# Kernel tuning notes

Measured on AMD Instinct MI355X. Metric: run time of the kernel, lower is better.

## Reference

```python
import jax, jax.numpy as jnp
import numpy as np

N = 16                      # input_dim (state dimension)
EPS = 1e-6
TRIL_R, TRIL_C = np.tril_indices(N)   # 136 lower-triangular slots


def setup_inputs() -> dict:
    key = jax.random.key(0)
    ks = jax.random.split(key, 7)
    B = 131072
    def xavier(k, fan_in, fan_out):
        lim = float(np.sqrt(6.0 / (fan_in + fan_out)))
        return jax.random.uniform(k, (fan_in, fan_out), jnp.float32, -lim, lim)
    return {
        "points": jax.random.normal(ks[0], (B, N), jnp.float32),
        "W0": xavier(ks[1], N, 512),
        "b0": jax.random.normal(ks[2], (512,), jnp.float32) * 0.01,
        "W1": xavier(ks[3], 512, 512),
        "b1": jax.random.normal(ks[4], (512,), jnp.float32) * 0.01,
        "W2": xavier(ks[5], 512, 136),
        "b2": jax.random.normal(ks[6], (136,), jnp.float32) * 0.01,
    }


def reference(points, W0, b0, W1, b1, W2, b2):
    # MLP: tanh, tanh, identity
    h = jnp.tanh(points @ W0 + b0)
    h = jnp.tanh(h @ W1 + b1)
    net = h @ W2 + b2                         # [B, 136] tril entries
    B = points.shape[0]
    # Batched scatter into lower-triangular matrices M: [B, N, N]
    M = jnp.zeros((B, N, N), points.dtype).at[:, TRIL_R, TRIL_C].set(net)
    # x^T (M M^T) x == ||M^T x||^2
    y = jnp.einsum('bij,bi->bj', M, points)   # (M^T x)_j = sum_i M_ij x_i
    vals = jnp.sum(y * y, axis=-1) + EPS * jnp.sum(points * points, axis=-1)
    return vals.reshape(-1, 1)
```

## Files before the change

kernel.cpp:

```cpp
#include <hip/hip_runtime.h>

typedef __bf16 bf16x4 __attribute__((ext_vector_type(4)));
typedef __bf16 bf16x8 __attribute__((ext_vector_type(8)));
typedef float f32x16 __attribute__((ext_vector_type(16)));

#define TC 2.885390081777926f

#define W0F_OFF 0
#define W1F_OFF 8192
#define W2F_OFF (8192 + 262144)

__global__ void prep_weights(const float* __restrict__ W0,
                             const float* __restrict__ W1,
                             const float* __restrict__ W2,
                             __bf16* __restrict__ ws) {
    const int wave = blockIdx.x * 8 + (threadIdx.x >> 6);
    const int l   = threadIdx.x & 63;
    const int col = l & 31, kh = l >> 5;
    const float* src; int nt, kk, S, nlim; float scl;
    if (wave < 16)       { src = W0; nt = wave; kk = 0;      S = 512; nlim = 512; scl = TC; }
    else if (wave < 528) { int r = wave - 16;  src = W1; nt = r >> 5; kk = r & 31; S = 512; nlim = 512; scl = TC; }
    else                 { int r = wave - 528; src = W2; nt = r >> 5; kk = r & 31; S = 136; nlim = 136; scl = 1.0f; }
    const int n  = nt * 32 + col;
    const int k0 = kk * 16 + kh * 8;
    bf16x8 v;
#pragma unroll
    for (int j = 0; j < 8; ++j)
        v[j] = (n < nlim) ? (__bf16)(src[(k0 + j) * S + n] * scl) : (__bf16)0.0f;
    *(bf16x8*)(ws + wave * 512 + l * 8) = v;
}

__device__ __forceinline__ float fast_tanh_pre(float y) {
#if __has_builtin(__builtin_amdgcn_exp2f)
    float e = __builtin_amdgcn_exp2f(y);
#else
    float e = exp2f(y);
#endif
    return 1.0f - 2.0f * __builtin_amdgcn_rcpf(e + 1.0f);
}

#define HSTR 520
#define NSTR 140

__global__ __launch_bounds__(512, 2)
void fused_mlp_quad(const float* __restrict__ points,
                    const float* __restrict__ b0,
                    const float* __restrict__ b1,
                    const float* __restrict__ b2,
                    const __bf16* __restrict__ ws,
                    float* __restrict__ out) {
    __shared__ __align__(16) unsigned char lds_raw[66560];
    __bf16* h  = (__bf16*)lds_raw;
    float* net = (float*)lds_raw;

    {
        const unsigned d = (blockIdx.x < 512)
                         ? ((blockIdx.x * 2654435761u) >> 29) : 0u;
        if (d > 0) __builtin_amdgcn_s_sleep(64);
        if (d > 1) __builtin_amdgcn_s_sleep(64);
        if (d > 2) __builtin_amdgcn_s_sleep(64);
        if (d > 3) __builtin_amdgcn_s_sleep(64);
        if (d > 4) __builtin_amdgcn_s_sleep(64);
        if (d > 5) __builtin_amdgcn_s_sleep(64);
        if (d > 6) __builtin_amdgcn_s_sleep(64);
    }

    const __bf16* w0f = ws + W0F_OFF;
    const __bf16* w1f = ws + W1F_OFF;
    const __bf16* w2f = ws + W2F_OFF;

    const int tid = threadIdx.x;
    const int w   = tid >> 6;
    const int l   = tid & 63;
    const int ln  = l & 31;
    const int hi  = l >> 5;
    const int row0 = blockIdx.x * 64;

    const int lofs = l * 8;
    const int ofs16 = (blockIdx.x >> 3) & 15;
    const int ofs8  = (blockIdx.x >> 3) & 7;

    {
        bf16x8 bx[2];
#pragma unroll
        for (int bt = 0; bt < 2; ++bt) {
            const float* src = points + (row0 + bt * 32 + ln) * 16 + hi * 8;
            float4 p0 = ((const float4*)src)[0];
            float4 p1 = ((const float4*)src)[1];
            bf16x8 v;
            v[0] = (__bf16)p0.x; v[1] = (__bf16)p0.y; v[2] = (__bf16)p0.z; v[3] = (__bf16)p0.w;
            v[4] = (__bf16)p1.x; v[5] = (__bf16)p1.y; v[6] = (__bf16)p1.z; v[7] = (__bf16)p1.w;
            bx[bt] = v;
        }
#pragma unroll
        for (int t = 0; t < 2; ++t) {
            const int ntg = w * 2 + t;
            bf16x8 wf = *(const bf16x8*)(w0f + ntg * 512 + lofs);
#pragma unroll
            for (int bt = 0; bt < 2; ++bt) {
                f32x16 acc = {};
                acc = __builtin_amdgcn_mfma_f32_32x32x16_bf16(wf, bx[bt], acc, 0, 0, 0);
#pragma unroll
                for (int rg = 0; rg < 4; ++rg) {
                    const int n0 = ntg * 32 + 8 * rg + 4 * hi;
                    float4 bias = *(const float4*)(b0 + n0);
                    bf16x4 v;
                    v[0] = (__bf16)fast_tanh_pre(fmaf(TC, bias.x, acc[4 * rg + 0]));
                    v[1] = (__bf16)fast_tanh_pre(fmaf(TC, bias.y, acc[4 * rg + 1]));
                    v[2] = (__bf16)fast_tanh_pre(fmaf(TC, bias.z, acc[4 * rg + 2]));
                    v[3] = (__bf16)fast_tanh_pre(fmaf(TC, bias.w, acc[4 * rg + 3]));
                    *(bf16x4*)(h + (bt * 32 + ln) * HSTR + n0) = v;
                }
            }
        }
    }
    __syncthreads();

    f32x16 acc1[2][2] = {};
    {
        const __bf16* arow0 = h + ln * HSTR + hi * 8;
        const __bf16* arow1 = h + (32 + ln) * HSTR + hi * 8;
        const __bf16* wb0 = w1f + (w * 2 + 0) * 16384 + lofs;
        const __bf16* wb1 = w1f + (w * 2 + 1) * 16384 + lofs;
        for (int ks2 = 0; ks2 < 16; ++ks2) {
            const int ks = (ks2 + ofs16) & 15;
            bf16x8 aa[2][2], bb[2][2];
#pragma unroll
            for (int u = 0; u < 2; ++u) {
                const int kk = ks * 2 + u;
                const int vo = kk * 512;
                aa[u][0] = *(const bf16x8*)(arow0 + kk * 16);
                aa[u][1] = *(const bf16x8*)(arow1 + kk * 16);
                bb[u][0] = *(const bf16x8*)(wb0 + vo);
                bb[u][1] = *(const bf16x8*)(wb1 + vo);
            }
#pragma unroll
            for (int u = 0; u < 2; ++u) {
#pragma unroll
                for (int t = 0; t < 2; ++t) {
                    acc1[0][t] = __builtin_amdgcn_mfma_f32_32x32x16_bf16(bb[u][t], aa[u][0], acc1[0][t], 0, 0, 0);
                    acc1[1][t] = __builtin_amdgcn_mfma_f32_32x32x16_bf16(bb[u][t], aa[u][1], acc1[1][t], 0, 0, 0);
                }
            }
        }
    }
    __syncthreads();
#pragma unroll
    for (int t = 0; t < 2; ++t) {
#pragma unroll
        for (int bt = 0; bt < 2; ++bt) {
#pragma unroll
            for (int rg = 0; rg < 4; ++rg) {
                const int n0 = (w * 2 + t) * 32 + 8 * rg + 4 * hi;
                float4 bias = *(const float4*)(b1 + n0);
                bf16x4 v;
                v[0] = (__bf16)fast_tanh_pre(fmaf(TC, bias.x, acc1[bt][t][4 * rg + 0]));
                v[1] = (__bf16)fast_tanh_pre(fmaf(TC, bias.y, acc1[bt][t][4 * rg + 1]));
                v[2] = (__bf16)fast_tanh_pre(fmaf(TC, bias.z, acc1[bt][t][4 * rg + 2]));
                v[3] = (__bf16)fast_tanh_pre(fmaf(TC, bias.w, acc1[bt][t][4 * rg + 3]));
                *(bf16x4*)(h + (bt * 32 + ln) * HSTR + n0) = v;
            }
        }
    }
    __syncthreads();

    f32x16 acc2a = {}, acc2e = {};
    const int nt2 = w >> 1;
    const int bt2 = w & 1;
    const bool two = (w < 2);
    {
        const __bf16* arowA = h + (bt2 * 32 + ln) * HSTR + hi * 8;
        const __bf16* arowE = h + ((w & 1) * 32 + ln) * HSTR + hi * 8;
        const __bf16* wbA = w2f + nt2 * 16384 + lofs;
        const __bf16* wbE = w2f + 4 * 16384 + lofs;
        for (int ks2 = 0; ks2 < 8; ++ks2) {
            const int ks = (ks2 + ofs8) & 7;
            bf16x8 aaA[2], wA[2], aaE[2], wE[2];
#pragma unroll
            for (int u = 0; u < 2; ++u) {
                const int kk = ks * 4 + u * 2;
                const int vo = kk * 512;
                aaA[u] = *(const bf16x8*)(arowA + kk * 16);
                wA[u]  = *(const bf16x8*)(wbA + vo);
                if (two) {
                    aaE[u] = *(const bf16x8*)(arowE + kk * 16);
                    wE[u]  = *(const bf16x8*)(wbE + vo);
                }
            }
            bf16x8 aaA2[2], wA2[2], aaE2[2], wE2[2];
#pragma unroll
            for (int u = 0; u < 2; ++u) {
                const int kk = ks * 4 + u * 2 + 1;
                const int vo = kk * 512;
                aaA2[u] = *(const bf16x8*)(arowA + kk * 16);
                wA2[u]  = *(const bf16x8*)(wbA + vo);
                if (two) {
                    aaE2[u] = *(const bf16x8*)(arowE + kk * 16);
                    wE2[u]  = *(const bf16x8*)(wbE + vo);
                }
            }
#pragma unroll
            for (int u = 0; u < 2; ++u) {
                acc2a = __builtin_amdgcn_mfma_f32_32x32x16_bf16(wA[u], aaA[u], acc2a, 0, 0, 0);
                acc2a = __builtin_amdgcn_mfma_f32_32x32x16_bf16(wA2[u], aaA2[u], acc2a, 0, 0, 0);
                if (two) {
                    acc2e = __builtin_amdgcn_mfma_f32_32x32x16_bf16(wE[u], aaE[u], acc2e, 0, 0, 0);
                    acc2e = __builtin_amdgcn_mfma_f32_32x32x16_bf16(wE2[u], aaE2[u], acc2e, 0, 0, 0);
                }
            }
        }
    }
    __syncthreads();
    {
#pragma unroll
        for (int rg = 0; rg < 4; ++rg) {
            const int n0 = nt2 * 32 + 8 * rg + 4 * hi;
            float4 bias = *(const float4*)(b2 + n0);
            float4 v;
            v.x = acc2a[4 * rg + 0] + bias.x;
            v.y = acc2a[4 * rg + 1] + bias.y;
            v.z = acc2a[4 * rg + 2] + bias.z;
            v.w = acc2a[4 * rg + 3] + bias.w;
            *(float4*)(net + (bt2 * 32 + ln) * NSTR + n0) = v;
        }
        if (two) {
            const int n0 = 128 + 4 * hi;
            float4 bias = *(const float4*)(b2 + n0);
            float4 v;
            v.x = acc2e[0] + bias.x;
            v.y = acc2e[1] + bias.y;
            v.z = acc2e[2] + bias.z;
            v.w = acc2e[3] + bias.w;
            *(float4*)(net + ((w & 1) * 32 + ln) * NSTR + n0) = v;
        }
    }
    __syncthreads();

    {
        const int r  = tid >> 3;
        const int jg = tid & 7;
        const float* xp = points + (row0 + r) * 16;
        float xv[16];
#pragma unroll
        for (int i = 0; i < 4; ++i) {
            float4 v = ((const float4*)xp)[i];
            xv[i * 4 + 0] = v.x; xv[i * 4 + 1] = v.y;
            xv[i * 4 + 2] = v.z; xv[i * 4 + 3] = v.w;
        }
        float sumsq = 0.f;
#pragma unroll
        for (int i = 0; i < 16; ++i) sumsq += xv[i] * xv[i];
        float p = 0.f;
#pragma unroll
        for (int jj = 0; jj < 2; ++jj) {
            const int j = jg + jj * 8;
            float y = 0.f;
#pragma unroll
            for (int i = 0; i < 16; ++i) {
                float mv = net[r * NSTR + ((i * (i + 1)) >> 1) + j];
                y += (i >= j) ? mv * xv[i] : 0.f;
            }
            p += y * y;
        }
        p += __shfl_xor(p, 1);
        p += __shfl_xor(p, 2);
        p += __shfl_xor(p, 4);
        if (jg == 0) out[row0 + r] = p + 1e-6f * sumsq;
    }
}

extern "C" void kernel_launch(void* const* d_in, const int* in_sizes, int n_in,
                              void* d_out, int out_size, void* d_ws, size_t ws_size,
                              hipStream_t stream) {
    const float* points = (const float*)d_in[0];
    const float* W0 = (const float*)d_in[1];
    const float* b0 = (const float*)d_in[2];
    const float* W1 = (const float*)d_in[3];
    const float* b1 = (const float*)d_in[4];
    const float* W2 = (const float*)d_in[5];
    const float* b2 = (const float*)d_in[6];
    __bf16* ws = (__bf16*)d_ws;
    float* out = (float*)d_out;

    prep_weights<<<86, 512, 0, stream>>>(W0, W1, W2, ws);

    const int B = in_sizes[0] / 16;
    fused_mlp_quad<<<B / 64, 512, 0, stream>>>(points, b0, b1, b2, ws, out);
}
```

Baseline: 196.8 us.

## Swizzle hidden-activation LDS layout with XOR and drop staggered start sleeps

```diff
diff --git a/kernel.cpp b/kernel.cpp
--- a/kernel.cpp
+++ b/kernel.cpp
@@ -53,18 +53,6 @@
     __bf16* h  = (__bf16*)lds_raw;
     float* net = (float*)lds_raw;
 
-    {
-        const unsigned d = (blockIdx.x < 512)
-                         ? ((blockIdx.x * 2654435761u) >> 29) : 0u;
-        if (d > 0) __builtin_amdgcn_s_sleep(64);
-        if (d > 1) __builtin_amdgcn_s_sleep(64);
-        if (d > 2) __builtin_amdgcn_s_sleep(64);
-        if (d > 3) __builtin_amdgcn_s_sleep(64);
-        if (d > 4) __builtin_amdgcn_s_sleep(64);
-        if (d > 5) __builtin_amdgcn_s_sleep(64);
-        if (d > 6) __builtin_amdgcn_s_sleep(64);
-    }
-
     const __bf16* w0f = ws + W0F_OFF;
     const __bf16* w1f = ws + W1F_OFF;
     const __bf16* w2f = ws + W2F_OFF;
@@ -79,6 +67,9 @@
     const int lofs = l * 8;
     const int ofs16 = (blockIdx.x >> 3) & 15;
     const int ofs8  = (blockIdx.x >> 3) & 7;
+
+    const int kq   = (ln >> 3) & 3;
+    const int hswz = kq << 4;
 
     {
         bf16x8 bx[2];
@@ -109,7 +100,7 @@
                     v[1] = (__bf16)fast_tanh_pre(fmaf(TC, bias.y, acc[4 * rg + 1]));
                     v[2] = (__bf16)fast_tanh_pre(fmaf(TC, bias.z, acc[4 * rg + 2]));
                     v[3] = (__bf16)fast_tanh_pre(fmaf(TC, bias.w, acc[4 * rg + 3]));
-                    *(bf16x4*)(h + (bt * 32 + ln) * HSTR + n0) = v;
+                    *(bf16x4*)(h + (bt * 32 + ln) * HSTR + (n0 ^ hswz)) = v;
                 }
             }
         }
@@ -128,9 +119,10 @@
 #pragma unroll
             for (int u = 0; u < 2; ++u) {
                 const int kk = ks * 2 + u;
+                const int kx = kk ^ kq;
                 const int vo = kk * 512;
-                aa[u][0] = *(const bf16x8*)(arow0 + kk * 16);
-                aa[u][1] = *(const bf16x8*)(arow1 + kk * 16);
+                aa[u][0] = *(const bf16x8*)(arow0 + kx * 16);
+                aa[u][1] = *(const bf16x8*)(arow1 + kx * 16);
                 bb[u][0] = *(const bf16x8*)(wb0 + vo);
                 bb[u][1] = *(const bf16x8*)(wb1 + vo);
             }
@@ -158,7 +150,7 @@
                 v[1] = (__bf16)fast_tanh_pre(fmaf(TC, bias.y, acc1[bt][t][4 * rg + 1]));
                 v[2] = (__bf16)fast_tanh_pre(fmaf(TC, bias.z, acc1[bt][t][4 * rg + 2]));
                 v[3] = (__bf16)fast_tanh_pre(fmaf(TC, bias.w, acc1[bt][t][4 * rg + 3]));
-                *(bf16x4*)(h + (bt * 32 + ln) * HSTR + n0) = v;
+                *(bf16x4*)(h + (bt * 32 + ln) * HSTR + (n0 ^ hswz)) = v;
             }
         }
     }
@@ -179,11 +171,12 @@
 #pragma unroll
             for (int u = 0; u < 2; ++u) {
                 const int kk = ks * 4 + u * 2;
+                const int kx = kk ^ kq;
                 const int vo = kk * 512;
-                aaA[u] = *(const bf16x8*)(arowA + kk * 16);
+                aaA[u] = *(const bf16x8*)(arowA + kx * 16);
                 wA[u]  = *(const bf16x8*)(wbA + vo);
                 if (two) {
-                    aaE[u] = *(const bf16x8*)(arowE + kk * 16);
+                    aaE[u] = *(const bf16x8*)(arowE + kx * 16);
                     wE[u]  = *(const bf16x8*)(wbE + vo);
                 }
             }
@@ -191,11 +184,12 @@
 #pragma unroll
             for (int u = 0; u < 2; ++u) {
                 const int kk = ks * 4 + u * 2 + 1;
+                const int kx = kk ^ kq;
                 const int vo = kk * 512;
-                aaA2[u] = *(const bf16x8*)(arowA + kk * 16);
+                aaA2[u] = *(const bf16x8*)(arowA + kx * 16);
                 wA2[u]  = *(const bf16x8*)(wbA + vo);
                 if (two) {
-                    aaE2[u] = *(const bf16x8*)(arowE + kk * 16);
+                    aaE2[u] = *(const bf16x8*)(arowE + kx * 16);
                     wE2[u]  = *(const bf16x8*)(wbE + vo);
                 }
             }
```

Measured after the change: 195.6 us. No clear change (-0.6%).

## Replicate W1 fragments across workspace copies and drop startup sleep staggering

Applied to the files above, without the earlier changes.

```diff
diff --git a/kernel.cpp b/kernel.cpp
--- a/kernel.cpp
+++ b/kernel.cpp
@@ -8,26 +8,27 @@
 
 #define W0F_OFF 0
 #define W1F_OFF 8192
-#define W2F_OFF (8192 + 262144)
+#define W1SZ    262144
 
 __global__ void prep_weights(const float* __restrict__ W0,
                              const float* __restrict__ W1,
                              const float* __restrict__ W2,
-                             __bf16* __restrict__ ws) {
+                             __bf16* __restrict__ ws, int rep) {
     const int wave = blockIdx.x * 8 + (threadIdx.x >> 6);
     const int l   = threadIdx.x & 63;
     const int col = l & 31, kh = l >> 5;
+    const int nW1 = rep * 512;
     const float* src; int nt, kk, S, nlim; float scl;
-    if (wave < 16)       { src = W0; nt = wave; kk = 0;      S = 512; nlim = 512; scl = TC; }
-    else if (wave < 528) { int r = wave - 16;  src = W1; nt = r >> 5; kk = r & 31; S = 512; nlim = 512; scl = TC; }
-    else                 { int r = wave - 528; src = W2; nt = r >> 5; kk = r & 31; S = 136; nlim = 136; scl = 1.0f; }
+    if (wave < 16)            { src = W0; nt = wave; kk = 0; S = 512; nlim = 512; scl = TC; }
+    else if (wave < 16 + nW1) { int r = (wave - 16) & 511;  src = W1; nt = r >> 5; kk = r & 31; S = 512; nlim = 512; scl = TC; }
+    else                      { int r = wave - 16 - nW1;    src = W2; nt = r >> 5; kk = r & 31; S = 136; nlim = 136; scl = 1.0f; }
     const int n  = nt * 32 + col;
     const int k0 = kk * 16 + kh * 8;
     bf16x8 v;
 #pragma unroll
     for (int j = 0; j < 8; ++j)
         v[j] = (n < nlim) ? (__bf16)(src[(k0 + j) * S + n] * scl) : (__bf16)0.0f;
-    *(bf16x8*)(ws + wave * 512 + l * 8) = v;
+    *(bf16x8*)(ws + (long)wave * 512 + l * 8) = v;
 }
 
 __device__ __forceinline__ float fast_tanh_pre(float y) {
@@ -48,26 +49,14 @@
                     const float* __restrict__ b1,
                     const float* __restrict__ b2,
                     const __bf16* __restrict__ ws,
-                    float* __restrict__ out) {
+                    float* __restrict__ out, int rep) {
     __shared__ __align__(16) unsigned char lds_raw[66560];
     __bf16* h  = (__bf16*)lds_raw;
     float* net = (float*)lds_raw;
 
-    {
-        const unsigned d = (blockIdx.x < 512)
-                         ? ((blockIdx.x * 2654435761u) >> 29) : 0u;
-        if (d > 0) __builtin_amdgcn_s_sleep(64);
-        if (d > 1) __builtin_amdgcn_s_sleep(64);
-        if (d > 2) __builtin_amdgcn_s_sleep(64);
-        if (d > 3) __builtin_amdgcn_s_sleep(64);
-        if (d > 4) __builtin_amdgcn_s_sleep(64);
-        if (d > 5) __builtin_amdgcn_s_sleep(64);
-        if (d > 6) __builtin_amdgcn_s_sleep(64);
-    }
-
     const __bf16* w0f = ws + W0F_OFF;
-    const __bf16* w1f = ws + W1F_OFF;
-    const __bf16* w2f = ws + W2F_OFF;
+    const __bf16* w1f = ws + W1F_OFF + (long)((blockIdx.x >> 3) & (rep - 1)) * W1SZ;
+    const __bf16* w2f = ws + W1F_OFF + (long)rep * W1SZ;
 
     const int tid = threadIdx.x;
     const int w   = tid >> 6;
@@ -282,8 +271,14 @@
     __bf16* ws = (__bf16*)d_ws;
     float* out = (float*)d_out;
 
-    prep_weights<<<86, 512, 0, stream>>>(W0, W1, W2, ws);
+    int rep = 1;
+    if (ws_size >= (size_t)(8192 + 8 * W1SZ + 81920) * 2) rep = 8;
+    else if (ws_size >= (size_t)(8192 + 4 * W1SZ + 81920) * 2) rep = 4;
+    else if (ws_size >= (size_t)(8192 + 2 * W1SZ + 81920) * 2) rep = 2;
+
+    const int prep_waves = 16 + rep * 512 + 160;
+    prep_weights<<<prep_waves / 8, 512, 0, stream>>>(W0, W1, W2, ws, rep);
 
     const int B = in_sizes[0] / 16;
-    fused_mlp_quad<<<B / 64, 512, 0, stream>>>(points, b0, b1, b2, ws, out);
-}
+    fused_mlp_quad<<<B / 64, 512, 0, stream>>>(points, b0, b1, b2, ws, out, rep);
+}
```

New measurement: 195.3 us. About the same (-0.8%).
